# Optimization experiments

Hardware: AMD Instinct MI355X
Metric: run time of the kernel (lower is better)

## Reference

```python
import jax, jax.numpy as jnp
import numpy as np

SEQ_LEN = 4096
INPUT_SIZE = 1024
OUTPUT_SIZE = 1024


def _xavier(key, shape):
    n = shape[0]
    lim = 1.0 / (n ** 0.5)
    return jax.random.uniform(key, shape, minval=-lim, maxval=lim, dtype=jnp.float32)


def setup_inputs() -> dict:
    key = jax.random.key(0)
    kx, kk, kv, kq = jax.random.split(key, 4)
    X = jax.random.normal(kx, (SEQ_LEN, INPUT_SIZE), dtype=jnp.float32)
    Wk = _xavier(kk, (INPUT_SIZE, OUTPUT_SIZE))
    Wv = _xavier(kv, (INPUT_SIZE, OUTPUT_SIZE))
    Wq = _xavier(kq, (INPUT_SIZE, OUTPUT_SIZE))
    return {"X": X, "Wk": Wk, "Wv": Wv, "Wq": Wq}


def reference(X, Wk, Wv, Wq):
    # Faithful to original: scores = K @ Q^T (note K first, no 1/sqrt(d) scaling)
    K = X @ Wk  # (S, D)
    V = X @ Wv  # (S, D)
    Q = X @ Wq  # (S, D)
    scores = jnp.einsum('sd,td->st', K, Q)  # (S, S) == K @ Q^T
    attn = jax.nn.softmax(scores, axis=-1) @ V  # (S, D)
    return attn
```

## Files before the change

kernel.cpp:

```cpp
#include <hip/hip_runtime.h>
#include <hip/hip_fp16.h>
#include <cstdint>

#define SEQ 4096
#define DIM 1024

typedef _Float16 f16x8 __attribute__((ext_vector_type(8)));
typedef float f32x16 __attribute__((ext_vector_type(16)));
typedef __attribute__((address_space(1))) void as1_void;
typedef __attribute__((address_space(3))) void as3_void;

__device__ __forceinline__ ushort f2h(float f) {
  _Float16 h = (_Float16)f;
  return __builtin_bit_cast(ushort, h);
}

__global__ void convert_all_kernel(const float* __restrict__ X, const float* __restrict__ Wk,
                                   const float* __restrict__ Wv, const float* __restrict__ Wq,
                                   ushort* __restrict__ Xh, ushort* __restrict__ Wt) {
  const int z = blockIdx.z;
  const int tx = threadIdx.x, ty = threadIdx.y;
  if (z == 3) {
    const int bid = blockIdx.y * 32 + blockIdx.x;
    const int t = ty * 32 + tx;
#pragma unroll
    for (int k = 0; k < 4; k++) {
      int i = bid * 1024 + k * 256 + t;
      float4 v = reinterpret_cast<const float4*>(X)[i];
      ushort4 o = { f2h(v.x), f2h(v.y), f2h(v.z), f2h(v.w) };
      reinterpret_cast<ushort4*>(Xh)[i] = o;
    }
    return;
  }
  __shared__ float tile[32][33];
  const float* W = (z == 0) ? Wk : (z == 1) ? Wv : Wq;
  int n0 = blockIdx.x * 32, k0 = blockIdx.y * 32;
#pragma unroll
  for (int r = 0; r < 4; r++) {
    int k = ty + r * 8;
    tile[k][tx] = W[(size_t)(k0 + k) * DIM + n0 + tx];
  }
  __syncthreads();
  ushort* out = Wt + (size_t)z * DIM * DIM;
#pragma unroll
  for (int r = 0; r < 4; r++) {
    int n = ty + r * 8;
    out[(size_t)(n0 + n) * DIM + k0 + tx] = f2h(tile[tx][n]);
  }
}

__device__ __forceinline__ void gemm512(const ushort* __restrict__ A,
                                        const ushort* __restrict__ B,
                                        ushort* __restrict__ C,
                                        int N, int K, int m0, int n0,
                                        int kt0, int ktend) {
  constexpr int BK = 64;
  __shared__ __align__(16) ushort As[2][256 * BK];
  __shared__ __align__(16) ushort Bs[2][256 * BK];
  const int tid = threadIdx.x;
  const int wave = tid >> 6, lane = tid & 63;
  const int l31 = lane & 31, khalf = lane >> 5;
  const int wm = (wave & 3) * 64, wn = (wave >> 2) * 128;

  const int srow = tid >> 3;
  const int skey = (srow & 7) ^ ((srow >> 3) & 3);
  const int sce = (((tid & 7) ^ skey) * 8);
  const int rk = (l31 & 7) ^ ((l31 >> 3) & 3);

  const ushort* Abase = A + (size_t)(m0 + srow) * K + sce;
  const ushort* Bbase = B + (size_t)(n0 + srow) * K + sce;

  f32x16 acc[2][4];
#pragma unroll
  for (int i = 0; i < 2; i++)
#pragma unroll
    for (int j = 0; j < 4; j++)
#pragma unroll
      for (int r = 0; r < 16; r++) acc[i][j][r] = 0.f;

  const int niter = (ktend - kt0) / BK;

#pragma unroll
  for (int q = 0; q < 4; q++) {
    __builtin_amdgcn_global_load_lds((const as1_void*)(Abase + (size_t)q * 64 * K + kt0),
                                     (as3_void*)&As[0][wave * 512 + q * 4096], 16, 0, 0);
    __builtin_amdgcn_global_load_lds((const as1_void*)(Bbase + (size_t)q * 64 * K + kt0),
                                     (as3_void*)&Bs[0][wave * 512 + q * 4096], 16, 0, 0);
  }

  for (int it = 0; it < niter; ++it) {
    __syncthreads();
    if (it + 1 < niter) {
      const int kt = kt0 + (it + 1) * BK;
      const int nb = (it + 1) & 1;
#pragma unroll
      for (int q = 0; q < 4; q++) {
        __builtin_amdgcn_global_load_lds((const as1_void*)(Abase + (size_t)q * 64 * K + kt),
                                         (as3_void*)&As[nb][wave * 512 + q * 4096], 16, 0, 0);
        __builtin_amdgcn_global_load_lds((const as1_void*)(Bbase + (size_t)q * 64 * K + kt),
                                         (as3_void*)&Bs[nb][wave * 512 + q * 4096], 16, 0, 0);
      }
    }
    const int cb = it & 1;
#pragma unroll
    for (int ks = 0; ks < 4; ks++) {
      f16x8 af[2], bfr[4];
      const int ck = (ks * 2 + khalf);
#pragma unroll
      for (int i = 0; i < 2; i++)
        af[i] = *reinterpret_cast<const f16x8*>(
            &As[cb][(wm + i * 32 + l31) * BK + ((ck ^ rk) * 8)]);
#pragma unroll
      for (int j = 0; j < 4; j++)
        bfr[j] = *reinterpret_cast<const f16x8*>(
            &Bs[cb][(wn + j * 32 + l31) * BK + ((ck ^ rk) * 8)]);
#pragma unroll
      for (int i = 0; i < 2; i++)
#pragma unroll
        for (int j = 0; j < 4; j++)
          acc[i][j] = __builtin_amdgcn_mfma_f32_32x32x16_f16(af[i], bfr[j], acc[i][j], 0, 0, 0);
    }
  }

#pragma unroll
  for (int i = 0; i < 2; i++)
#pragma unroll
    for (int j = 0; j < 4; j++)
#pragma unroll
      for (int r = 0; r < 16; r++) {
        int row = m0 + wm + i * 32 + (r & 3) + 8 * (r >> 2) + 4 * khalf;
        int col = n0 + wn + j * 32 + l31;
        C[(size_t)row * N + col] = f2h(acc[i][j][r]);
      }
}

__global__ __launch_bounds__(512, 2) void proj_kernel(const ushort* __restrict__ Xh,
                                                      const ushort* __restrict__ Wt,
                                                      ushort* __restrict__ Kh,
                                                      ushort* __restrict__ Qh,
                                                      ushort* __restrict__ Vt) {
  const int z = blockIdx.z;
  const int bx = blockIdx.x;
  if (z < 2) {
    const ushort* B = Wt + (size_t)(z == 0 ? 0 : 2) * DIM * DIM;
    ushort* C = (z == 0) ? Kh : Qh;
    gemm512(Xh, B, C, DIM, DIM, (bx >> 2) * 256, (bx & 3) * 256, 0, DIM);
  } else {
    gemm512(Wt + (size_t)DIM * DIM, Xh, Vt, SEQ, DIM,
            (bx >> 4) * 256, (bx & 15) * 256, 0, DIM);
  }
}

__global__ __launch_bounds__(512, 2) void score_kernel(const ushort* __restrict__ Kh,
                                                       const ushort* __restrict__ Qh,
                                                       ushort* __restrict__ S) {
  const int f = blockIdx.x;
  const int xcd = f & 7;
  const int r = f >> 3;
  const int g = xcd * 2 + (r >> 4);
  const int w = r & 15;
  const int sx = w & 3, sy = w >> 2;
  const int tx = (g & 3) * 4 + sx;
  const int ty = (g >> 2) * 4 + sy;
  gemm512(Kh, Qh, S, SEQ, DIM, ty * 256, tx * 256, 0, DIM);
}

__global__ __launch_bounds__(512, 2) void out_splitk_kernel(const ushort* __restrict__ P,
                                                            const ushort* __restrict__ Vt,
                                                            ushort* __restrict__ Part) {
  const int f = blockIdx.x;
  const int xcd = f & 7;
  const int r = f >> 3;
  const int z = r >> 3;
  const int u = r & 7;
  const int t = xcd * 8 + u;
  const int ty = t >> 2, tx = t & 3;
  ushort* C = Part + (size_t)z * SEQ * DIM;
  gemm512(P, Vt, C, DIM, SEQ, ty * 256, tx * 256,
          z * (SEQ / 4), (z + 1) * (SEQ / 4));
}

__global__ void reduce4_kernel(const ushort* __restrict__ Part, float* __restrict__ out, int n8) {
  int i = blockIdx.x * blockDim.x + threadIdx.x;
  if (i >= n8) return;
  const f16x8* p0 = reinterpret_cast<const f16x8*>(Part);
  const f16x8* p1 = p0 + n8;
  const f16x8* p2 = p1 + n8;
  const f16x8* p3 = p2 + n8;
  f16x8 a = p0[i], b = p1[i], c = p2[i], d = p3[i];
  float4 lo, hi;
  lo.x = (float)a[0] + (float)b[0] + (float)c[0] + (float)d[0];
  lo.y = (float)a[1] + (float)b[1] + (float)c[1] + (float)d[1];
  lo.z = (float)a[2] + (float)b[2] + (float)c[2] + (float)d[2];
  lo.w = (float)a[3] + (float)b[3] + (float)c[3] + (float)d[3];
  hi.x = (float)a[4] + (float)b[4] + (float)c[4] + (float)d[4];
  hi.y = (float)a[5] + (float)b[5] + (float)c[5] + (float)d[5];
  hi.z = (float)a[6] + (float)b[6] + (float)c[6] + (float)d[6];
  hi.w = (float)a[7] + (float)b[7] + (float)c[7] + (float)d[7];
  reinterpret_cast<float4*>(out)[i * 2] = lo;
  reinterpret_cast<float4*>(out)[i * 2 + 1] = hi;
}

__global__ __launch_bounds__(256) void softmax_kernel(const ushort* __restrict__ S,
                                                      ushort* __restrict__ P) {
  const int wave = threadIdx.x >> 6, lane = threadIdx.x & 63;
  const int row = blockIdx.x * 4 + wave;
  const ushort* s = S + (size_t)row * SEQ;
  float v[64];
#pragma unroll
  for (int i = 0; i < 8; i++) {
    f16x8 h = reinterpret_cast<const f16x8*>(s)[i * 64 + lane];
#pragma unroll
    for (int j = 0; j < 8; j++) v[i * 8 + j] = (float)h[j];
  }
  float m = v[0];
#pragma unroll
  for (int j = 1; j < 64; j++) m = fmaxf(m, v[j]);
#pragma unroll
  for (int o = 32; o > 0; o >>= 1) m = fmaxf(m, __shfl_xor(m, o, 64));
  float sum = 0.f;
#pragma unroll
  for (int j = 0; j < 64; j++) {
    v[j] = __expf(v[j] - m);
    sum += v[j];
  }
#pragma unroll
  for (int o = 32; o > 0; o >>= 1) sum += __shfl_xor(sum, o, 64);
  float inv = 1.0f / sum;
  ushort* p = P + (size_t)row * SEQ;
#pragma unroll
  for (int i = 0; i < 8; i++) {
    f16x8 h;
#pragma unroll
    for (int j = 0; j < 8; j++) h[j] = (_Float16)(v[i * 8 + j] * inv);
    reinterpret_cast<f16x8*>(p)[i * 64 + lane] = h;
  }
}

extern "C" void kernel_launch(void* const* d_in, const int* in_sizes, int n_in,
                              void* d_out, int out_size, void* d_ws, size_t ws_size,
                              hipStream_t stream) {
  const float* X = (const float*)d_in[0];
  const float* Wk = (const float*)d_in[1];
  const float* Wv = (const float*)d_in[2];
  const float* Wq = (const float*)d_in[3];

  char* ws = (char*)d_ws;
  size_t off = 0;
  ushort* Xh = (ushort*)(ws + off); off += (size_t)SEQ * DIM * 2;
  ushort* Wt = (ushort*)(ws + off); off += (size_t)3 * DIM * DIM * 2;
  ushort* Kh = (ushort*)(ws + off); off += (size_t)SEQ * DIM * 2;
  ushort* Qh = (ushort*)(ws + off); off += (size_t)SEQ * DIM * 2;
  ushort* Vt = (ushort*)(ws + off); off += (size_t)SEQ * DIM * 2;
  ushort* S = (ushort*)(ws + off);  off += (size_t)SEQ * SEQ * 2;
  ushort* P = (ushort*)(ws + off);  off += (size_t)SEQ * SEQ * 2;

  ushort* Part = S;

  convert_all_kernel<<<dim3(32, 32, 4), dim3(32, 8), 0, stream>>>(X, Wk, Wv, Wq, Xh, Wt);
  proj_kernel<<<dim3(64, 1, 3), 512, 0, stream>>>(Xh, Wt, Kh, Qh, Vt);
  score_kernel<<<256, 512, 0, stream>>>(Kh, Qh, S);
  softmax_kernel<<<1024, 256, 0, stream>>>(S, P);
  out_splitk_kernel<<<256, 512, 0, stream>>>(P, Vt, Part);
  reduce4_kernel<<<SEQ * DIM / 8 / 256, 256, 0, stream>>>(Part, (float*)d_out, SEQ * DIM / 8);
}
```

Measured before the change: 210.2 us.

## Shrink GEMM tiles to 128x128 with two waves and single-buffered LDS

Replaces the 256x256, 8-wave, double-buffered GEMM helper with a 128x128, 2-wave version that uses one LDS buffer, synchronises before and after each K-slab load, and recomputes the swizzle per row. All three GEMM launches (projection, score, split-K output) now use four times as many 128-thread blocks, with the XCD-aware tile remapping adjusted to match. The aim is more blocks and waves resident per CU and better load balance. In exchange, each block reuses loaded tiles across less work, so global and L2 traffic per FLOP rises, and global loads no longer overlap with MFMA compute.

```diff
diff --git a/kernel.cpp b/kernel.cpp
--- a/kernel.cpp
+++ b/kernel.cpp
@@ -49,27 +49,22 @@
   }
 }
 
-__device__ __forceinline__ void gemm512(const ushort* __restrict__ A,
+__device__ __forceinline__ void gemm128(const ushort* __restrict__ A,
                                         const ushort* __restrict__ B,
                                         ushort* __restrict__ C,
                                         int N, int K, int m0, int n0,
                                         int kt0, int ktend) {
   constexpr int BK = 64;
-  __shared__ __align__(16) ushort As[2][256 * BK];
-  __shared__ __align__(16) ushort Bs[2][256 * BK];
+  __shared__ __align__(16) ushort As[128 * BK];
+  __shared__ __align__(16) ushort Bs[128 * BK];
   const int tid = threadIdx.x;
   const int wave = tid >> 6, lane = tid & 63;
   const int l31 = lane & 31, khalf = lane >> 5;
-  const int wm = (wave & 3) * 64, wn = (wave >> 2) * 128;
+  const int wm = wave * 64;
 
   const int srow = tid >> 3;
-  const int skey = (srow & 7) ^ ((srow >> 3) & 3);
-  const int sce = (((tid & 7) ^ skey) * 8);
   const int rk = (l31 & 7) ^ ((l31 >> 3) & 3);
 
-  const ushort* Abase = A + (size_t)(m0 + srow) * K + sce;
-  const ushort* Bbase = B + (size_t)(n0 + srow) * K + sce;
-
   f32x16 acc[2][4];
 #pragma unroll
   for (int i = 0; i < 2; i++)
@@ -78,42 +73,35 @@
 #pragma unroll
       for (int r = 0; r < 16; r++) acc[i][j][r] = 0.f;
 
-  const int niter = (ktend - kt0) / BK;
-
-#pragma unroll
-  for (int q = 0; q < 4; q++) {
-    __builtin_amdgcn_global_load_lds((const as1_void*)(Abase + (size_t)q * 64 * K + kt0),
-                                     (as3_void*)&As[0][wave * 512 + q * 4096], 16, 0, 0);
-    __builtin_amdgcn_global_load_lds((const as1_void*)(Bbase + (size_t)q * 64 * K + kt0),
-                                     (as3_void*)&Bs[0][wave * 512 + q * 4096], 16, 0, 0);
-  }
-
-  for (int it = 0; it < niter; ++it) {
+  for (int kt = kt0; kt < ktend; kt += BK) {
     __syncthreads();
-    if (it + 1 < niter) {
-      const int kt = kt0 + (it + 1) * BK;
-      const int nb = (it + 1) & 1;
-#pragma unroll
-      for (int q = 0; q < 4; q++) {
-        __builtin_amdgcn_global_load_lds((const as1_void*)(Abase + (size_t)q * 64 * K + kt),
-                                         (as3_void*)&As[nb][wave * 512 + q * 4096], 16, 0, 0);
-        __builtin_amdgcn_global_load_lds((const as1_void*)(Bbase + (size_t)q * 64 * K + kt),
-                                         (as3_void*)&Bs[nb][wave * 512 + q * 4096], 16, 0, 0);
-      }
-    }
-    const int cb = it & 1;
+#pragma unroll
+    for (int q = 0; q < 8; q++) {
+      const int row = q * 16 + srow;
+      const int key = (row & 7) ^ ((row >> 3) & 3);
+      const int ce = ((tid & 7) ^ key) * 8;
+      __builtin_amdgcn_global_load_lds((const as1_void*)(A + (size_t)(m0 + row) * K + kt + ce),
+                                       (as3_void*)&As[q * 1024 + wave * 512], 16, 0, 0);
+    }
+#pragma unroll
+    for (int q = 0; q < 8; q++) {
+      const int row = q * 16 + srow;
+      const int key = (row & 7) ^ ((row >> 3) & 3);
+      const int ce = ((tid & 7) ^ key) * 8;
+      __builtin_amdgcn_global_load_lds((const as1_void*)(B + (size_t)(n0 + row) * K + kt + ce),
+                                       (as3_void*)&Bs[q * 1024 + wave * 512], 16, 0, 0);
+    }
+    __syncthreads();
 #pragma unroll
     for (int ks = 0; ks < 4; ks++) {
       f16x8 af[2], bfr[4];
-      const int ck = (ks * 2 + khalf);
+      const int co = ((ks * 2 + khalf) ^ rk) * 8;
 #pragma unroll
       for (int i = 0; i < 2; i++)
-        af[i] = *reinterpret_cast<const f16x8*>(
-            &As[cb][(wm + i * 32 + l31) * BK + ((ck ^ rk) * 8)]);
+        af[i] = *reinterpret_cast<const f16x8*>(&As[(wm + i * 32 + l31) * BK + co]);
 #pragma unroll
       for (int j = 0; j < 4; j++)
-        bfr[j] = *reinterpret_cast<const f16x8*>(
-            &Bs[cb][(wn + j * 32 + l31) * BK + ((ck ^ rk) * 8)]);
+        bfr[j] = *reinterpret_cast<const f16x8*>(&Bs[(j * 32 + l31) * BK + co]);
 #pragma unroll
       for (int i = 0; i < 2; i++)
 #pragma unroll
@@ -129,12 +117,12 @@
 #pragma unroll
       for (int r = 0; r < 16; r++) {
         int row = m0 + wm + i * 32 + (r & 3) + 8 * (r >> 2) + 4 * khalf;
-        int col = n0 + wn + j * 32 + l31;
+        int col = n0 + j * 32 + l31;
         C[(size_t)row * N + col] = f2h(acc[i][j][r]);
       }
 }
 
-__global__ __launch_bounds__(512, 2) void proj_kernel(const ushort* __restrict__ Xh,
+__global__ __launch_bounds__(128, 2) void proj_kernel(const ushort* __restrict__ Xh,
                                                       const ushort* __restrict__ Wt,
                                                       ushort* __restrict__ Kh,
                                                       ushort* __restrict__ Qh,
@@ -144,39 +132,39 @@
   if (z < 2) {
     const ushort* B = Wt + (size_t)(z == 0 ? 0 : 2) * DIM * DIM;
     ushort* C = (z == 0) ? Kh : Qh;
-    gemm512(Xh, B, C, DIM, DIM, (bx >> 2) * 256, (bx & 3) * 256, 0, DIM);
+    gemm128(Xh, B, C, DIM, DIM, (bx >> 3) * 128, (bx & 7) * 128, 0, DIM);
   } else {
-    gemm512(Wt + (size_t)DIM * DIM, Xh, Vt, SEQ, DIM,
-            (bx >> 4) * 256, (bx & 15) * 256, 0, DIM);
-  }
-}
-
-__global__ __launch_bounds__(512, 2) void score_kernel(const ushort* __restrict__ Kh,
+    gemm128(Wt + (size_t)DIM * DIM, Xh, Vt, SEQ, DIM,
+            (bx >> 5) * 128, (bx & 31) * 128, 0, DIM);
+  }
+}
+
+__global__ __launch_bounds__(128, 2) void score_kernel(const ushort* __restrict__ Kh,
                                                        const ushort* __restrict__ Qh,
                                                        ushort* __restrict__ S) {
   const int f = blockIdx.x;
   const int xcd = f & 7;
   const int r = f >> 3;
-  const int g = xcd * 2 + (r >> 4);
-  const int w = r & 15;
-  const int sx = w & 3, sy = w >> 2;
-  const int tx = (g & 3) * 4 + sx;
-  const int ty = (g >> 2) * 4 + sy;
-  gemm512(Kh, Qh, S, SEQ, DIM, ty * 256, tx * 256, 0, DIM);
-}
-
-__global__ __launch_bounds__(512, 2) void out_splitk_kernel(const ushort* __restrict__ P,
+  const int t = xcd * 128 + r;
+  const int st = t >> 6, within = t & 63;
+  const int sx = within & 7, sy = within >> 3;
+  const int tx = (st & 3) * 8 + sx;
+  const int ty = (st >> 2) * 8 + sy;
+  gemm128(Kh, Qh, S, SEQ, DIM, ty * 128, tx * 128, 0, DIM);
+}
+
+__global__ __launch_bounds__(128, 2) void out_splitk_kernel(const ushort* __restrict__ P,
                                                             const ushort* __restrict__ Vt,
                                                             ushort* __restrict__ Part) {
   const int f = blockIdx.x;
-  const int xcd = f & 7;
-  const int r = f >> 3;
-  const int z = r >> 3;
-  const int u = r & 7;
-  const int t = xcd * 8 + u;
-  const int ty = t >> 2, tx = t & 3;
+  const int z = f >> 8;
+  const int q = f & 255;
+  const int xcd = q & 7;
+  const int r = q >> 3;
+  const int t = xcd * 32 + r;
+  const int ty = t >> 3, tx = t & 7;
   ushort* C = Part + (size_t)z * SEQ * DIM;
-  gemm512(P, Vt, C, DIM, SEQ, ty * 256, tx * 256,
+  gemm128(P, Vt, C, DIM, SEQ, ty * 128, tx * 128,
           z * (SEQ / 4), (z + 1) * (SEQ / 4));
 }
 
@@ -258,9 +246,9 @@
   ushort* Part = S;
 
   convert_all_kernel<<<dim3(32, 32, 4), dim3(32, 8), 0, stream>>>(X, Wk, Wv, Wq, Xh, Wt);
-  proj_kernel<<<dim3(64, 1, 3), 512, 0, stream>>>(Xh, Wt, Kh, Qh, Vt);
-  score_kernel<<<256, 512, 0, stream>>>(Kh, Qh, S);
+  proj_kernel<<<dim3(256, 1, 3), 128, 0, stream>>>(Xh, Wt, Kh, Qh, Vt);
+  score_kernel<<<1024, 128, 0, stream>>>(Kh, Qh, S);
   softmax_kernel<<<1024, 256, 0, stream>>>(S, P);
-  out_splitk_kernel<<<256, 512, 0, stream>>>(P, Vt, Part);
+  out_splitk_kernel<<<1024, 128, 0, stream>>>(P, Vt, Part);
   reduce4_kernel<<<SEQ * DIM / 8 / 256, 256, 0, stream>>>(Part, (float*)d_out, SEQ * DIM / 8);
 }
```

Measured after the change: 214.7 us. +2.1%, slower.
